# Kernel optimization log

Hardware: AMD Instinct MI355X
Metric: run time of the kernel (lower is better)

The kernel has to match this reference:

```python
import jax, jax.numpy as jnp
import numpy as np

B, N, DIM, H = 4, 2048, 1024, 16
HEAD_DIM = DIM // H
SCALE = HEAD_DIM ** (-0.5)


def setup_inputs() -> dict:
    key = jax.random.key(0)
    k1, k2, k3 = jax.random.split(key, 3)
    x = jax.random.normal(k1, (B, N, DIM), dtype=jnp.float32)
    # nn.Linear(dim, 3*dim, bias=False): weight shape [3*dim, dim], y = x @ W.T
    w_qkv = jax.random.normal(k2, (3 * DIM, DIM), dtype=jnp.float32) * 0.02
    w_proj = jax.random.normal(k3, (DIM, DIM), dtype=jnp.float32) * 0.02
    return {"x": x, "w_qkv": w_qkv, "w_proj": w_proj}


def reference(x, w_qkv, w_proj):
    Bv, Nv, C = x.shape
    Dh = C // H
    # qkv projection -> [B, N, 3, H, Dh]
    qkv = (x @ w_qkv.T).reshape(Bv, Nv, 3, H, Dh)
    q, k, v = qkv[:, :, 0], qkv[:, :, 1], qkv[:, :, 2]  # each [B, N, H, Dh]
    # scaled dot-product attention per head (online-softmax loop collapses to this)
    scores = jnp.einsum("bnhd,bmhd->bhnm", q, k) * SCALE  # [B, H, N, N]
    attn = jax.nn.softmax(scores, axis=-1)
    out = jnp.einsum("bhnm,bmhd->bnhd", attn, v).reshape(Bv, Nv, C)
    return out @ w_proj.T
```

## Files before the change

### kernel.cpp

```cpp
#include <hip/hip_runtime.h>

typedef __bf16 bf16;
typedef bf16 bf16x8 __attribute__((ext_vector_type(8)));
typedef float f32x4 __attribute__((ext_vector_type(4)));
typedef float f32x16 __attribute__((ext_vector_type(16)));
typedef int i32x2 __attribute__((ext_vector_type(2)));

#define B_   4
#define N_   2048
#define DIM_ 1024
#define H_   16
#define DH_  64
#define M_   (B_ * N_)

#define CEXP 0.18033688f

#define GLOBAL_CP(g) (const __attribute__((address_space(1))) void*)(g)
#define LDS_CP(l)    (__attribute__((address_space(3))) void*)(l)

__global__ __launch_bounds__(256) void cvt_all(
    const float* __restrict__ x, const float* __restrict__ wq,
    const float* __restrict__ wp, bf16* __restrict__ o,
    int nx4, int nwq4, int nwp4)
{
    const int i = blockIdx.x * blockDim.x + threadIdx.x;
    const float* src; int si;
    if (i < nx4)                { src = x;  si = i; }
    else if (i < nx4 + nwq4)    { src = wq; si = i - nx4; }
    else                        { src = wp; si = i - nx4 - nwq4; }
    const float4 v = ((const float4*)src)[si];
    union { bf16 h[4]; uint2 u; } r;
    r.h[0] = (bf16)v.x; r.h[1] = (bf16)v.y;
    r.h[2] = (bf16)v.z; r.h[3] = (bf16)v.w;
    ((uint2*)o)[i] = r.u;
}

__global__ __launch_bounds__(256) void gemm_bt(
    const bf16* __restrict__ A, const bf16* __restrict__ Bm,
    int Ndim, int K, int mode,
    float* __restrict__ outf,
    bf16* __restrict__ qb, bf16* __restrict__ kbv, bf16* __restrict__ vbT)
{
    __shared__ bf16 As[128 * 64];
    __shared__ bf16 Bs[128 * 64];

    const int tid  = threadIdx.x;
    const int wave = tid >> 6;
    const int lane = tid & 63;
    const int quad = lane >> 4;
    const int lr   = lane & 15;
    const int wr   = wave >> 1, wc = wave & 1;
    const int m0 = blockIdx.y * 128;
    const int n0 = blockIdx.x * 128;

    f32x4 acc[4][4];
#pragma unroll
    for (int i = 0; i < 4; i++)
#pragma unroll
        for (int j = 0; j < 4; j++) acc[i][j] = f32x4{0.f, 0.f, 0.f, 0.f};

    const int sl8 = lane >> 3;
    const int sc8 = ((lane & 7) ^ (sl8 & 7)) * 8;

    for (int k0 = 0; k0 < K; k0 += 64) {
        __syncthreads();
#pragma unroll
        for (int c = 0; c < 4; c++) {
            const int ii  = wave * 4 + c;
            const int row = ii * 8 + sl8;
            __builtin_amdgcn_global_load_lds(
                GLOBAL_CP(A + (size_t)(m0 + row) * K + k0 + sc8),
                LDS_CP(&As[ii * 512 + lane * 8]), 16, 0, 0);
            __builtin_amdgcn_global_load_lds(
                GLOBAL_CP(Bm + (size_t)(n0 + row) * K + k0 + sc8),
                LDS_CP(&Bs[ii * 512 + lane * 8]), 16, 0, 0);
        }
        __syncthreads();

#pragma unroll
        for (int s = 0; s < 2; s++) {
            bf16x8 af[4], bfr[4];
#pragma unroll
            for (int i = 0; i < 4; i++) {
                const int R = wr * 64 + i * 16 + lr;
                af[i] = *(const bf16x8*)(&As[R * 64 + (((s * 4 + quad) ^ (R & 7)) << 3)]);
            }
#pragma unroll
            for (int j = 0; j < 4; j++) {
                const int R = wc * 64 + j * 16 + lr;
                bfr[j] = *(const bf16x8*)(&Bs[R * 64 + (((s * 4 + quad) ^ (R & 7)) << 3)]);
            }
#pragma unroll
            for (int i = 0; i < 4; i++)
#pragma unroll
                for (int j = 0; j < 4; j++)
                    acc[i][j] = __builtin_amdgcn_mfma_f32_16x16x32_bf16(
                        af[i], bfr[j], acc[i][j], 0, 0, 0);
        }
    }

#pragma unroll
    for (int i = 0; i < 4; i++) {
        const int mbase = m0 + wr * 64 + i * 16 + quad * 4;
#pragma unroll
        for (int j = 0; j < 4; j++) {
            const int n = n0 + wc * 64 + j * 16 + lr;
            if (mode == 0) {
#pragma unroll
                for (int r = 0; r < 4; r++)
                    outf[(size_t)(mbase + r) * Ndim + n] = acc[i][j][r];
            } else {
                const int which = n >> 10;
                const int h = (n >> 6) & 15;
                const int d = n & 63;
                const int b  = mbase >> 11;
                const int t0 = mbase & 2047;
                if (which == 2) {
                    union { uint2 u; bf16 hh[4]; } p;
#pragma unroll
                    for (int r = 0; r < 4; r++) p.hh[r] = (bf16)acc[i][j][r];
                    *(uint2*)(&vbT[(((size_t)(b * 16 + h)) * 64 + d) * 2048 + t0]) = p.u;
                } else {
                    bf16* dst = (which == 0) ? qb : kbv;
                    const float sc = (which == 0) ? CEXP : 1.0f;
#pragma unroll
                    for (int r = 0; r < 4; r++)
                        dst[(((size_t)(b * 16 + h)) * 2048 + t0 + r) * 64 + d] =
                            (bf16)(acc[i][j][r] * sc);
                }
            }
        }
    }
}

__global__ __launch_bounds__(256, 4) void attn_kernel(
    const bf16* __restrict__ qb, const bf16* __restrict__ kb,
    const bf16* __restrict__ vbT, bf16* __restrict__ ao)
{
    __shared__ bf16 Ks[2][32 * 128];
    __shared__ bf16 Vs[2][32 * 128];

    const int tid  = threadIdx.x;
    const int wave = tid >> 6;
    const int lane = tid & 63;
    const int l31  = lane & 31;
    const int hh   = lane >> 5;

    const int bid = blockIdx.x;
    const int qt  = (bid >> 3) & 15;
    const int bh  = ((bid >> 7) << 3) | (bid & 7);

    const bf16* Q  = qb  + (size_t)bh * N_ * DH_;
    const bf16* Kp = kb  + (size_t)bh * N_ * DH_;
    const bf16* Vp = vbT + (size_t)bh * DH_ * N_;

    bf16x8 qf[4];
#pragma unroll
    for (int ks = 0; ks < 4; ks++)
        qf[ks] = *(const bf16x8*)(Q + (size_t)(qt * 128 + wave * 32 + l31) * DH_
                                    + ks * 16 + hh * 8);

    bf16x8 onesb;
#pragma unroll
    for (int j = 0; j < 8; j++) onesb[j] = (bf16)1.0f;

    const int sr = lane >> 4;
    const int sp = lane & 15;

    f32x16 oacc[2];
    f32x16 sacc;
#pragma unroll
    for (int r = 0; r < 16; r++) { oacc[0][r] = 0.f; oacc[1][r] = 0.f; sacc[r] = 0.f; }

#define STAGE(t, pb)                                                          \
    do {                                                                      \
        _Pragma("unroll")                                                     \
        for (int c2 = 0; c2 < 2; c2++) {                                      \
            const int ii = wave * 2 + c2;                           \
            const int rr = ii * 4 + sr;                            \
            const int lc = sp ^ (rr & 15);                 \
            const int kk = 2 * rr + (lc >> 3);           \
            const int d0 = (lc & 7) * 8;               \
            __builtin_amdgcn_global_load_lds(                                 \
                GLOBAL_CP(Kp + (size_t)((t) * 64 + kk) * DH_ + d0),           \
                LDS_CP(&Ks[pb][ii * 512 + lane * 8]), 16, 0, 0);              \
            __builtin_amdgcn_global_load_lds(                                 \
                GLOBAL_CP(Vp + (size_t)kk * N_ + (t) * 64 + d0),              \
                LDS_CP(&Vs[pb][ii * 512 + lane * 8]), 16, 0, 0);              \
        }                                                                     \
    } while (0)

    STAGE(0, 0);
    __syncthreads();

    int cur = 0;
    for (int t = 0; t < N_ / 64; t++) {
        if (t + 1 < N_ / 64) STAGE(t + 1, cur ^ 1);

#pragma unroll
        for (int kbk = 0; kbk < 2; kbk++) {
            f32x16 e;
#pragma unroll
            for (int r = 0; r < 16; r++) e[r] = 0.f;
            __builtin_amdgcn_s_setprio(1);
#pragma unroll
            for (int ks = 0; ks < 4; ks++) {
                const int R  = kbk * 32 + l31;
                const int rr = R >> 1;
                const int ch = ks * 2 + hh;
                const int pc = (((R & 1) << 3) | ch) ^ (rr & 15);
                bf16x8 ak = *(const bf16x8*)(&Ks[cur][rr * 128 + pc * 8]);
                e = __builtin_amdgcn_mfma_f32_32x32x16_bf16(ak, qf[ks], e, 0, 0, 0);
            }
            __builtin_amdgcn_s_setprio(0);

            bf16x8 bv[2][2];
#pragma unroll
            for (int dblk = 0; dblk < 2; dblk++) {
#pragma unroll
                for (int half = 0; half < 2; half++) {
                    const int Rv  = dblk * 32 + l31;
                    const int rv  = Rv >> 1;
                    const int chv = kbk * 4 + half * 2 + hh;
                    const int pv_ = (((Rv & 1) << 3) | chv) ^ (rv & 15);
                    bv[dblk][half] = *(const bf16x8*)(&Vs[cur][rv * 128 + pv_ * 8]);
                }
            }

#pragma unroll
            for (int r = 0; r < 16; r++) e[r] = __builtin_amdgcn_exp2f(e[r]);

            uint g[8];
#pragma unroll
            for (int m = 0; m < 8; m++) {
                union { uint u; bf16 h2[2]; } pk;
                pk.h2[0] = (bf16)e[2 * m];
                pk.h2[1] = (bf16)e[2 * m + 1];
                g[m] = pk.u;
            }

            const i32x2 s0 = __builtin_amdgcn_permlane32_swap((int)g[0], (int)g[2], false, false);
            const i32x2 s1 = __builtin_amdgcn_permlane32_swap((int)g[1], (int)g[3], false, false);
            const i32x2 s2 = __builtin_amdgcn_permlane32_swap((int)g[4], (int)g[6], false, false);
            const i32x2 s3 = __builtin_amdgcn_permlane32_swap((int)g[5], (int)g[7], false, false);

            union { uint u[4]; bf16x8 v; } p0u, p1u;
            p0u.u[0] = (uint)s0[0];
            p0u.u[1] = (uint)s1[0];
            p0u.u[2] = (uint)s0[1];
            p0u.u[3] = (uint)s1[1];
            p1u.u[0] = (uint)s2[0];
            p1u.u[1] = (uint)s3[0];
            p1u.u[2] = (uint)s2[1];
            p1u.u[3] = (uint)s3[1];

            __builtin_amdgcn_s_setprio(1);
            sacc = __builtin_amdgcn_mfma_f32_32x32x16_bf16(p0u.v, onesb, sacc, 0, 0, 0);
            sacc = __builtin_amdgcn_mfma_f32_32x32x16_bf16(p1u.v, onesb, sacc, 0, 0, 0);

#pragma unroll
            for (int dblk = 0; dblk < 2; dblk++) {
                oacc[dblk] = __builtin_amdgcn_mfma_f32_32x32x16_bf16(p0u.v, bv[dblk][0], oacc[dblk], 0, 0, 0);
                oacc[dblk] = __builtin_amdgcn_mfma_f32_32x32x16_bf16(p1u.v, bv[dblk][1], oacc[dblk], 0, 0, 0);
            }
            __builtin_amdgcn_s_setprio(0);
        }

        __syncthreads();
        cur ^= 1;
    }
#undef STAGE

    const int head = bh & 15;
    const int b    = bh >> 4;
#pragma unroll
    for (int r = 0; r < 16; r++) {
        const int qr  = (r & 3) + 8 * (r >> 2) + 4 * hh;
        const float inv = 1.0f / sacc[r];
        const int qrow = qt * 128 + wave * 32 + qr;
#pragma unroll
        for (int dblk = 0; dblk < 2; dblk++)
            ao[((size_t)(b * 2048 + qrow)) * 1024 + head * 64 + dblk * 32 + l31] =
                (bf16)(oacc[dblk][r] * inv);
    }
}

extern "C" void kernel_launch(void* const* d_in, const int* in_sizes, int n_in,
                              void* d_out, int out_size, void* d_ws, size_t ws_size,
                              hipStream_t stream)
{
    const float* x     = (const float*)d_in[0];
    const float* wqkv  = (const float*)d_in[1];
    const float* wproj = (const float*)d_in[2];
    float* out = (float*)d_out;

    const size_t nx  = (size_t)M_ * DIM_;
    const size_t nwq = (size_t)3 * DIM_ * DIM_;
    const size_t nwp = (size_t)DIM_ * DIM_;
    const size_t seg = (size_t)B_ * H_ * N_ * DH_;

    bf16* xb     = (bf16*)d_ws;
    bf16* wqkvb  = xb + nx;
    bf16* wprojb = wqkvb + nwq;
    bf16* qb     = wprojb + nwp;
    bf16* kb     = qb + seg;
    bf16* vbT    = kb + seg;
    bf16* ao     = xb;

    const int nx4  = (int)(nx / 4), nwq4 = (int)(nwq / 4), nwp4 = (int)(nwp / 4);
    cvt_all<<<(nx4 + nwq4 + nwp4) / 256, 256, 0, stream>>>(
        x, wqkv, wproj, xb, nx4, nwq4, nwp4);

    gemm_bt<<<dim3(24, 64), 256, 0, stream>>>(xb, wqkvb, 3 * DIM_, DIM_, 1,
                                              nullptr, qb, kb, vbT);
    attn_kernel<<<dim3(1024), 256, 0, stream>>>(qb, kb, vbT, ao);
    gemm_bt<<<dim3(8, 64), 256, 0, stream>>>(ao, wprojb, DIM_, DIM_, 0,
                                             out, nullptr, nullptr, nullptr);
}
```

Measured before the change: 279.2 us.

## Replace ones-MFMA row sums with VALU sums and precompute LDS offsets

Each lane now adds its exp values on the VALU, and the two half-wave partials are combined with a shuffle, replacing the two extra MFMAs per key block that multiplied P by a ones matrix to get the softmax denominators. The normalizer is broadcast back to the output layout with __shfl. LDS read offsets and global/LDS staging addresses are precomputed and advanced incrementally. The loop is unrolled by two so the double-buffer offset is a compile-time constant. This trades MFMA work for VALU adds and shuffles and adds address registers, which could raise register pressure.

After: 275.5 us. No clear change (-1.3%).

```diff
diff --git a/kernel.cpp b/kernel.cpp
--- a/kernel.cpp
+++ b/kernel.cpp
@@ -160,123 +160,153 @@
         qf[ks] = *(const bf16x8*)(Q + (size_t)(qt * 128 + wave * 32 + l31) * DH_
                                     + ks * 16 + hh * 8);
 
-    bf16x8 onesb;
-#pragma unroll
-    for (int j = 0; j < 8; j++) onesb[j] = (bf16)1.0f;
+    f32x16 kZ;
+#pragma unroll
+    for (int r = 0; r < 16; r++) kZ[r] = 0.f;
+
+    int kofs[8];
+#pragma unroll
+    for (int kbk = 0; kbk < 2; kbk++)
+#pragma unroll
+        for (int ks = 0; ks < 4; ks++) {
+            const int R  = kbk * 32 + l31;
+            const int rr = R >> 1;
+            const int ch = ks * 2 + hh;
+            const int pc = (((R & 1) << 3) | ch) ^ (rr & 15);
+            kofs[kbk * 4 + ks] = rr * 256 + pc * 16;
+        }
+    int vofs[8];
+#pragma unroll
+    for (int kbk = 0; kbk < 2; kbk++)
+#pragma unroll
+        for (int dblk = 0; dblk < 2; dblk++)
+#pragma unroll
+            for (int half = 0; half < 2; half++) {
+                const int Rv  = dblk * 32 + l31;
+                const int rv  = Rv >> 1;
+                const int chv = kbk * 4 + half * 2 + hh;
+                const int pv_ = (((Rv & 1) << 3) | chv) ^ (rv & 15);
+                vofs[kbk * 4 + dblk * 2 + half] = rv * 256 + pv_ * 16;
+            }
 
     const int sr = lane >> 4;
     const int sp = lane & 15;
+    const bf16* ksrc[2];
+    const bf16* vsrc[2];
+    int sdst[2];
+#pragma unroll
+    for (int c2 = 0; c2 < 2; c2++) {
+        const int ii  = wave * 2 + c2;
+        const int rr2 = ii * 4 + sr;
+        const int lc  = sp ^ (rr2 & 15);
+        const int kk  = 2 * rr2 + (lc >> 3);
+        const int d0  = (lc & 7) * 8;
+        ksrc[c2] = Kp + (size_t)kk * DH_ + d0;
+        vsrc[c2] = Vp + (size_t)kk * N_ + d0;
+        sdst[c2] = ii * 1024 + lane * 16;
+    }
+
+    const char* ksB = (const char*)Ks;
+    const char* vsB = (const char*)Vs;
+    char* ksBm = (char*)Ks;
+    char* vsBm = (char*)Vs;
 
     f32x16 oacc[2];
-    f32x16 sacc;
-#pragma unroll
-    for (int r = 0; r < 16; r++) { oacc[0][r] = 0.f; oacc[1][r] = 0.f; sacc[r] = 0.f; }
-
-#define STAGE(t, pb)                                                          \
-    do {                                                                      \
+#pragma unroll
+    for (int r = 0; r < 16; r++) { oacc[0][r] = 0.f; oacc[1][r] = 0.f; }
+    float lrow = 0.f;
+
+#define STAGE()                                                               \
+    {                                                                         \
         _Pragma("unroll")                                                     \
         for (int c2 = 0; c2 < 2; c2++) {                                      \
-            const int ii = wave * 2 + c2;                           \
-            const int rr = ii * 4 + sr;                            \
-            const int lc = sp ^ (rr & 15);                 \
-            const int kk = 2 * rr + (lc >> 3);           \
-            const int d0 = (lc & 7) * 8;               \
-            __builtin_amdgcn_global_load_lds(                                 \
-                GLOBAL_CP(Kp + (size_t)((t) * 64 + kk) * DH_ + d0),           \
-                LDS_CP(&Ks[pb][ii * 512 + lane * 8]), 16, 0, 0);              \
-            __builtin_amdgcn_global_load_lds(                                 \
-                GLOBAL_CP(Vp + (size_t)kk * N_ + (t) * 64 + d0),              \
-                LDS_CP(&Vs[pb][ii * 512 + lane * 8]), 16, 0, 0);              \
+            __builtin_amdgcn_global_load_lds(GLOBAL_CP(ksrc[c2]),             \
+                LDS_CP(ksBm + sdst[c2]), 16, 0, 0);                           \
+            __builtin_amdgcn_global_load_lds(GLOBAL_CP(vsrc[c2]),             \
+                LDS_CP(vsBm + sdst[c2]), 16, 0, 0);                           \
+            ksrc[c2] += 64 * DH_;                 \
+            vsrc[c2] += 64;                      \
+            sdst[c2] ^= 8192;                           \
         }                                                                     \
-    } while (0)
-
-    STAGE(0, 0);
+    }
+
+#define TILE(BUFB)                                                            \
+    {                                                                         \
+        float ssum = 0.f;                                                     \
+        _Pragma("unroll")                                                     \
+        for (int kbk = 0; kbk < 2; kbk++) {                                   \
+            f32x16 e;                                                         \
+            __builtin_amdgcn_s_setprio(1);                                    \
+            _Pragma("unroll")                                                 \
+            for (int ks = 0; ks < 4; ks++) {                                  \
+                bf16x8 ak = *(const bf16x8*)(ksB + kofs[kbk * 4 + ks] + (BUFB)); \
+                e = __builtin_amdgcn_mfma_f32_32x32x16_bf16(                  \
+                        ak, qf[ks], ks == 0 ? kZ : e, 0, 0, 0);               \
+            }                                                                 \
+            __builtin_amdgcn_s_setprio(0);                                    \
+            bf16x8 bv[2][2];                                                  \
+            _Pragma("unroll")                                                 \
+            for (int dblk = 0; dblk < 2; dblk++)                              \
+                _Pragma("unroll")                                             \
+                for (int half = 0; half < 2; half++)                          \
+                    bv[dblk][half] = *(const bf16x8*)(                        \
+                        vsB + vofs[kbk * 4 + dblk * 2 + half] + (BUFB));      \
+            _Pragma("unroll")                                                 \
+            for (int r = 0; r < 16; r++) e[r] = __builtin_amdgcn_exp2f(e[r]); \
+            _Pragma("unroll")                                                 \
+            for (int r = 0; r < 16; r++) ssum += e[r];                        \
+            uint g[8];                                                        \
+            _Pragma("unroll")                                                 \
+            for (int m = 0; m < 8; m++) {                                     \
+                union { uint u; bf16 h2[2]; } pk;                             \
+                pk.h2[0] = (bf16)e[2 * m];                                    \
+                pk.h2[1] = (bf16)e[2 * m + 1];                                \
+                g[m] = pk.u;                                                  \
+            }                                                                 \
+            const i32x2 s0 = __builtin_amdgcn_permlane32_swap((int)g[0], (int)g[2], false, false); \
+            const i32x2 s1 = __builtin_amdgcn_permlane32_swap((int)g[1], (int)g[3], false, false); \
+            const i32x2 s2 = __builtin_amdgcn_permlane32_swap((int)g[4], (int)g[6], false, false); \
+            const i32x2 s3 = __builtin_amdgcn_permlane32_swap((int)g[5], (int)g[7], false, false); \
+            union { uint u[4]; bf16x8 v; } p0u, p1u;                          \
+            p0u.u[0] = (uint)s0[0]; p0u.u[1] = (uint)s1[0];                   \
+            p0u.u[2] = (uint)s0[1]; p0u.u[3] = (uint)s1[1];                   \
+            p1u.u[0] = (uint)s2[0]; p1u.u[1] = (uint)s3[0];                   \
+            p1u.u[2] = (uint)s2[1]; p1u.u[3] = (uint)s3[1];                   \
+            __builtin_amdgcn_s_setprio(1);                                    \
+            _Pragma("unroll")                                                 \
+            for (int dblk = 0; dblk < 2; dblk++) {                            \
+                oacc[dblk] = __builtin_amdgcn_mfma_f32_32x32x16_bf16(         \
+                    p0u.v, bv[dblk][0], oacc[dblk], 0, 0, 0);                 \
+                oacc[dblk] = __builtin_amdgcn_mfma_f32_32x32x16_bf16(         \
+                    p1u.v, bv[dblk][1], oacc[dblk], 0, 0, 0);                 \
+            }                                                                 \
+            __builtin_amdgcn_s_setprio(0);                                    \
+        }                                                                     \
+        ssum += __shfl_xor(ssum, 32);                                         \
+        lrow += ssum;                                                         \
+    }
+
+    STAGE();
     __syncthreads();
 
-    int cur = 0;
-    for (int t = 0; t < N_ / 64; t++) {
-        if (t + 1 < N_ / 64) STAGE(t + 1, cur ^ 1);
-
-#pragma unroll
-        for (int kbk = 0; kbk < 2; kbk++) {
-            f32x16 e;
-#pragma unroll
-            for (int r = 0; r < 16; r++) e[r] = 0.f;
-            __builtin_amdgcn_s_setprio(1);
-#pragma unroll
-            for (int ks = 0; ks < 4; ks++) {
-                const int R  = kbk * 32 + l31;
-                const int rr = R >> 1;
-                const int ch = ks * 2 + hh;
-                const int pc = (((R & 1) << 3) | ch) ^ (rr & 15);
-                bf16x8 ak = *(const bf16x8*)(&Ks[cur][rr * 128 + pc * 8]);
-                e = __builtin_amdgcn_mfma_f32_32x32x16_bf16(ak, qf[ks], e, 0, 0, 0);
-            }
-            __builtin_amdgcn_s_setprio(0);
-
-            bf16x8 bv[2][2];
-#pragma unroll
-            for (int dblk = 0; dblk < 2; dblk++) {
-#pragma unroll
-                for (int half = 0; half < 2; half++) {
-                    const int Rv  = dblk * 32 + l31;
-                    const int rv  = Rv >> 1;
-                    const int chv = kbk * 4 + half * 2 + hh;
-                    const int pv_ = (((Rv & 1) << 3) | chv) ^ (rv & 15);
-                    bv[dblk][half] = *(const bf16x8*)(&Vs[cur][rv * 128 + pv_ * 8]);
-                }
-            }
-
-#pragma unroll
-            for (int r = 0; r < 16; r++) e[r] = __builtin_amdgcn_exp2f(e[r]);
-
-            uint g[8];
-#pragma unroll
-            for (int m = 0; m < 8; m++) {
-                union { uint u; bf16 h2[2]; } pk;
-                pk.h2[0] = (bf16)e[2 * m];
-                pk.h2[1] = (bf16)e[2 * m + 1];
-                g[m] = pk.u;
-            }
-
-            const i32x2 s0 = __builtin_amdgcn_permlane32_swap((int)g[0], (int)g[2], false, false);
-            const i32x2 s1 = __builtin_amdgcn_permlane32_swap((int)g[1], (int)g[3], false, false);
-            const i32x2 s2 = __builtin_amdgcn_permlane32_swap((int)g[4], (int)g[6], false, false);
-            const i32x2 s3 = __builtin_amdgcn_permlane32_swap((int)g[5], (int)g[7], false, false);
-
-            union { uint u[4]; bf16x8 v; } p0u, p1u;
-            p0u.u[0] = (uint)s0[0];
-            p0u.u[1] = (uint)s1[0];
-            p0u.u[2] = (uint)s0[1];
-            p0u.u[3] = (uint)s1[1];
-            p1u.u[0] = (uint)s2[0];
-            p1u.u[1] = (uint)s3[0];
-            p1u.u[2] = (uint)s2[1];
-            p1u.u[3] = (uint)s3[1];
-
-            __builtin_amdgcn_s_setprio(1);
-            sacc = __builtin_amdgcn_mfma_f32_32x32x16_bf16(p0u.v, onesb, sacc, 0, 0, 0);
-            sacc = __builtin_amdgcn_mfma_f32_32x32x16_bf16(p1u.v, onesb, sacc, 0, 0, 0);
-
-#pragma unroll
-            for (int dblk = 0; dblk < 2; dblk++) {
-                oacc[dblk] = __builtin_amdgcn_mfma_f32_32x32x16_bf16(p0u.v, bv[dblk][0], oacc[dblk], 0, 0, 0);
-                oacc[dblk] = __builtin_amdgcn_mfma_f32_32x32x16_bf16(p1u.v, bv[dblk][1], oacc[dblk], 0, 0, 0);
-            }
-            __builtin_amdgcn_s_setprio(0);
-        }
-
+    for (int tt = 0; tt < 16; tt++) {
+        STAGE();
+        TILE(0);
         __syncthreads();
-        cur ^= 1;
+        if (tt < 15) STAGE();
+        TILE(8192);
+        __syncthreads();
     }
 #undef STAGE
+#undef TILE
 
     const int head = bh & 15;
     const int b    = bh >> 4;
+    const float linv = 1.0f / lrow;
 #pragma unroll
     for (int r = 0; r < 16; r++) {
         const int qr  = (r & 3) + 8 * (r >> 2) + 4 * hh;
-        const float inv = 1.0f / sacc[r];
+        const float inv = __shfl(linv, qr);
         const int qrow = qt * 128 + wave * 32 + qr;
 #pragma unroll
         for (int dblk = 0; dblk < 2; dblk++)
```

## Stage V transpose through LDS and compute softmax row sums with VALU

Applied to the files above, without the earlier changes.

In the QKV GEMM, blocks that produce V now write their bf16 tile into shared memory with a swizzle and read it back transposed, so the V^T stores become coalesced 16-byte writes instead of scattered 8-byte writes. In the attention kernel, the row-sum MFMA against a ones vector is replaced by per-lane VALU adds of the exponentials plus a cross-half shuffle, and the final normalisation fetches the inverse sum with a lane shuffle. This is meant to cut MFMA work and uncoalesced global stores. In exchange it adds VALU adds, extra LDS traffic and barriers in the GEMM epilogue, and it keeps the row sum in fp32 rather than summing bf16-rounded probabilities.

New measurement: 274.0 us. No clear change (-1.9%).

```diff
diff --git a/kernel.cpp b/kernel.cpp
--- a/kernel.cpp
+++ b/kernel.cpp
@@ -41,8 +41,9 @@
     float* __restrict__ outf,
     bf16* __restrict__ qb, bf16* __restrict__ kbv, bf16* __restrict__ vbT)
 {
-    __shared__ bf16 As[128 * 64];
-    __shared__ bf16 Bs[128 * 64];
+    __shared__ bf16 smem[128 * 128];
+    bf16* As = smem;
+    bf16* Bs = smem + 128 * 64;
 
     const int tid  = threadIdx.x;
     const int wave = tid >> 6;
@@ -99,6 +100,39 @@
         }
     }
 
+    if (mode == 1 && blockIdx.x >= 16) {
+        __syncthreads();
+        const int b    = m0 >> 11;
+        const int t0_0 = m0 & 2047;
+        const int h0   = (n0 - 2048) >> 6;
+#pragma unroll
+        for (int i = 0; i < 4; i++) {
+            const int c8 = wr * 16 + i * 4 + quad;
+#pragma unroll
+            for (int j = 0; j < 4; j++) {
+                const int dl = wc * 64 + j * 16 + lr;
+                const int p8 = c8 ^ (lr << 1);
+                union { uint2 u; bf16 hh[4]; } p;
+#pragma unroll
+                for (int r = 0; r < 4; r++) p.hh[r] = (bf16)acc[i][j][r];
+                *(uint2*)((char*)smem + dl * 256 + p8 * 8) = p.u;
+            }
+        }
+        __syncthreads();
+#pragma unroll
+        for (int k = 0; k < 8; k++) {
+            const int cid = k * 256 + tid;
+            const int row = cid >> 4;
+            const int c16 = cid & 15;
+            const uint4 v = *(const uint4*)((const char*)smem
+                                + row * 256 + ((c16 ^ (row & 15)) * 16));
+            bf16* dst = vbT + ((size_t)(b * 16 + h0 + (row >> 6)) * 64
+                               + (row & 63)) * 2048 + t0_0 + c16 * 8;
+            *(uint4*)dst = v;
+        }
+        return;
+    }
+
 #pragma unroll
     for (int i = 0; i < 4; i++) {
         const int mbase = m0 + wr * 64 + i * 16 + quad * 4;
@@ -110,24 +144,16 @@
                 for (int r = 0; r < 4; r++)
                     outf[(size_t)(mbase + r) * Ndim + n] = acc[i][j][r];
             } else {
-                const int which = n >> 10;
                 const int h = (n >> 6) & 15;
                 const int d = n & 63;
                 const int b  = mbase >> 11;
                 const int t0 = mbase & 2047;
-                if (which == 2) {
-                    union { uint2 u; bf16 hh[4]; } p;
-#pragma unroll
-                    for (int r = 0; r < 4; r++) p.hh[r] = (bf16)acc[i][j][r];
-                    *(uint2*)(&vbT[(((size_t)(b * 16 + h)) * 64 + d) * 2048 + t0]) = p.u;
-                } else {
-                    bf16* dst = (which == 0) ? qb : kbv;
-                    const float sc = (which == 0) ? CEXP : 1.0f;
-#pragma unroll
-                    for (int r = 0; r < 4; r++)
-                        dst[(((size_t)(b * 16 + h)) * 2048 + t0 + r) * 64 + d] =
-                            (bf16)(acc[i][j][r] * sc);
-                }
+                bf16* dst = (n < 1024) ? qb : kbv;
+                const float sc = (n < 1024) ? CEXP : 1.0f;
+#pragma unroll
+                for (int r = 0; r < 4; r++)
+                    dst[(((size_t)(b * 16 + h)) * 2048 + t0 + r) * 64 + d] =
+                        (bf16)(acc[i][j][r] * sc);
             }
         }
     }
@@ -160,17 +186,13 @@
         qf[ks] = *(const bf16x8*)(Q + (size_t)(qt * 128 + wave * 32 + l31) * DH_
                                     + ks * 16 + hh * 8);
 
-    bf16x8 onesb;
-#pragma unroll
-    for (int j = 0; j < 8; j++) onesb[j] = (bf16)1.0f;
-
     const int sr = lane >> 4;
     const int sp = lane & 15;
 
     f32x16 oacc[2];
-    f32x16 sacc;
-#pragma unroll
-    for (int r = 0; r < 16; r++) { oacc[0][r] = 0.f; oacc[1][r] = 0.f; sacc[r] = 0.f; }
+#pragma unroll
+    for (int r = 0; r < 16; r++) { oacc[0][r] = 0.f; oacc[1][r] = 0.f; }
+    float lrow = 0.f;
 
 #define STAGE(t, pb)                                                          \
     do {                                                                      \
@@ -197,6 +219,7 @@
     for (int t = 0; t < N_ / 64; t++) {
         if (t + 1 < N_ / 64) STAGE(t + 1, cur ^ 1);
 
+        float ssum = 0.f;
 #pragma unroll
         for (int kbk = 0; kbk < 2; kbk++) {
             f32x16 e;
@@ -229,6 +252,8 @@
 
 #pragma unroll
             for (int r = 0; r < 16; r++) e[r] = __builtin_amdgcn_exp2f(e[r]);
+#pragma unroll
+            for (int r = 0; r < 16; r++) ssum += e[r];
 
             uint g[8];
 #pragma unroll
@@ -255,9 +280,6 @@
             p1u.u[3] = (uint)s3[1];
 
             __builtin_amdgcn_s_setprio(1);
-            sacc = __builtin_amdgcn_mfma_f32_32x32x16_bf16(p0u.v, onesb, sacc, 0, 0, 0);
-            sacc = __builtin_amdgcn_mfma_f32_32x32x16_bf16(p1u.v, onesb, sacc, 0, 0, 0);
-
 #pragma unroll
             for (int dblk = 0; dblk < 2; dblk++) {
                 oacc[dblk] = __builtin_amdgcn_mfma_f32_32x32x16_bf16(p0u.v, bv[dblk][0], oacc[dblk], 0, 0, 0);
@@ -265,6 +287,8 @@
             }
             __builtin_amdgcn_s_setprio(0);
         }
+        ssum += __shfl_xor(ssum, 32);
+        lrow += ssum;
 
         __syncthreads();
         cur ^= 1;
@@ -273,10 +297,11 @@
 
     const int head = bh & 15;
     const int b    = bh >> 4;
+    const float linv = 1.0f / lrow;
 #pragma unroll
     for (int r = 0; r < 16; r++) {
         const int qr  = (r & 3) + 8 * (r >> 2) + 4 * hh;
-        const float inv = 1.0f / sacc[r];
+        const float inv = __shfl(linv, qr);
         const int qrow = qt * 128 + wave * 32 + qr;
 #pragma unroll
         for (int dblk = 0; dblk < 2; dblk++)
```
